# Kernel tuning notes

Hardware: AMD Instinct MI355X
Metric: run time of the kernel (lower is better)

The kernel has to match this reference:

```python
import jax, jax.numpy as jnp
import numpy as np

# Static module hyperparameters (from init_kwargs)
K = 4        # kernel_size
STRIDE = 2
L = 2        # n_layers
F = 4        # filters
NQ = 6       # n_qubits = ceil(log2(4*4*4)) = 6
D = 1 << NQ  # statevector dim = 64 = in_channels*K*K (no padding needed)

# Pauli-Z expectation sign table: wire 0 is the most-significant bit (PennyLane convention)
_bits = (jnp.arange(D)[None, :] >> (NQ - 1 - jnp.arange(NQ)[:, None])) & 1  # (NQ, D)
ZSIGNS = (1 - 2 * _bits).astype(jnp.float32)                                # (NQ, D)


def setup_inputs() -> dict:
    key = jax.random.key(0)
    k1, k2 = jax.random.split(key)
    x = jax.random.normal(k1, (128, 4, 64, 64), dtype=jnp.float32)
    weights = jax.random.normal(k2, (F, L, NQ, 3), dtype=jnp.float32)
    return {"x": x, "weights": weights}


def _rot_mat(phi, theta, omega):
    # qml.Rot = RZ(omega) @ RY(theta) @ RZ(phi)
    c = jnp.cos(theta / 2)
    s = jnp.sin(theta / 2)
    return jnp.stack([
        jnp.stack([jnp.exp(-1j * (phi + omega) / 2) * c, -jnp.exp(1j * (phi - omega) / 2) * s]),
        jnp.stack([jnp.exp(-1j * (phi - omega) / 2) * s, jnp.exp(1j * (phi + omega) / 2) * c]),
    ])  # (2,2) complex64


def _apply_1q(state, U, w):
    # state: (N, D) complex; apply 2x2 unitary on wire w (MSB-first ordering)
    N = state.shape[0]
    s = state.reshape(N, 1 << w, 2, 1 << (NQ - 1 - w))
    s = jnp.einsum('ij,najb->naib', U, s)
    return s.reshape(N, D)


def _apply_cnot(state, c, t):
    # flip target bit t where control bit c is 1
    N = state.shape[0]
    a, b = min(c, t), max(c, t)
    s = state.reshape(N, 1 << a, 2, 1 << (b - a - 1), 2, 1 << (NQ - 1 - b))
    if c < t:
        # control axis=2, target axis=4
        s = s.at[:, :, 1].set(s[:, :, 1, :, ::-1, :])
    else:
        # target axis=2, control axis=4
        s = s.at[:, :, :, :, 1, :].set(s[:, :, ::-1, :, 1, :])
    return s.reshape(N, D)


def _simulate(psi0, wf):
    # psi0: (N, D) complex64 normalized amplitudes; wf: (L, NQ, 3) float32
    state = psi0
    # The torch module applies StronglyEntanglingLayers(weights) L times -> L*L layers total.
    for _ in range(L):
        for l in range(L):
            for w in range(NQ):
                U = _rot_mat(wf[l, w, 0], wf[l, w, 1], wf[l, w, 2])
                state = _apply_1q(state, U, w)
            r = (l % (NQ - 1)) + 1  # StronglyEntanglingLayers default ranges
            for w in range(NQ):
                state = _apply_cnot(state, w, (w + r) % NQ)
    probs = state.real ** 2 + state.imag ** 2  # (N, D)
    return probs @ ZSIGNS.T                    # (N, NQ) Pauli-Z expvals


def reference(x, weights):
    B, C, H, W = x.shape
    oh = (H - K) // STRIDE + 1
    i = jnp.arange(oh) * STRIDE
    # vectorized sliding-window patch extraction, row-major (i outer, j inner)
    rows = x[:, :, i[:, None] + jnp.arange(K)[None, :], :]           # (B,C,oh,K,W)
    pat = rows[:, :, :, :, i[:, None] + jnp.arange(K)[None, :]]      # (B,C,oh,K,oh,K)
    pat = pat.transpose(0, 2, 4, 1, 3, 5).reshape(B, oh * oh, C * K * K)  # (B,P,D), flatten order (C,k,k)
    # AmplitudeEmbedding with normalize=True (C*K*K == 2**NQ, no padding)
    norm = jnp.linalg.norm(pat, axis=-1, keepdims=True)
    psi0 = (pat / norm).astype(jnp.complex64).reshape(-1, D)         # (B*P, D)
    exp = jax.vmap(lambda wf: _simulate(psi0, wf))(weights)          # (F, B*P, NQ)
    out = exp.reshape(F, B, oh * oh, NQ).transpose(1, 0, 3, 2).reshape(B, F * NQ, oh, oh)
    return out
```

## Files before the change

kernel.cpp:

```cpp
#include <hip/hip_runtime.h>

typedef float f32x2 __attribute__((ext_vector_type(2)));
typedef float f32x16 __attribute__((ext_vector_type(16)));
typedef __bf16 bf16x8 __attribute__((ext_vector_type(8)));

static __device__ __forceinline__ unsigned short f2bf(float v) {
    unsigned u = __builtin_bit_cast(unsigned, v);
    unsigned r = (u + 0x7FFFu + ((u >> 16) & 1u)) >> 16;
    return (unsigned short)r;
}
static __device__ __forceinline__ bf16x8 ldg8(const unsigned short* p) {
    uint4 u = *(const uint4*)p;
    return __builtin_bit_cast(bf16x8, u);
}
static __device__ __forceinline__ f32x16 mfma32(bf16x8 a, bf16x8 b, f32x16 c) {
    return __builtin_amdgcn_mfma_f32_32x32x16_bf16(a, b, c, 0, 0, 0);
}

__global__ __launch_bounds__(256) void prep_M(const float* __restrict__ wts,
                                              unsigned short* __restrict__ Mhi) {
    __shared__ float gls[12][8];
    const int f = blockIdx.x >> 4;
    const int tid = threadIdx.x;
    if (tid < 12) {
        int l = tid / 6, w = tid % 6;
        const float* p = wts + ((f * 2 + l) * 6 + w) * 3;
        float phi = p[0], theta = p[1], omega = p[2];
        float c, s; sincosf(0.5f * theta, &s, &c);
        float sapo, capo, samo, camo;
        sincosf(0.5f * (phi + omega), &sapo, &capo);
        sincosf(0.5f * (phi - omega), &samo, &camo);
        float* o = gls[tid];
        o[0] =  capo * c;  o[1] = -sapo * c;
        o[2] = -camo * s;  o[3] = -samo * s;
        o[4] =  camo * s;  o[5] = -samo * s;
        o[6] =  capo * c;  o[7] =  sapo * c;
    }
    __syncthreads();

    const int lane = tid & 63;
    const int wid  = tid >> 6;
    const int bas  = (blockIdx.x & 15) * 4 + wid;

    int src0 = lane, src1 = lane;
#pragma unroll
    for (int w = 5; w >= 0; --w) { int tq = (w + 1) % 6; src0 ^= ((src0 >> (5 - w)) & 1) << (5 - tq); }
#pragma unroll
    for (int w = 5; w >= 0; --w) { int tq = (w + 2) % 6; src1 ^= ((src1 >> (5 - w)) & 1) << (5 - tq); }

    float ar = (lane == bas) ? 1.0f : 0.0f, ai = 0.0f;
#pragma unroll
    for (int rep = 0; rep < 2; ++rep) {
#pragma unroll
        for (int l = 0; l < 2; ++l) {
#pragma unroll
            for (int w = 0; w < 6; ++w) {
                const float* gp = gls[l * 6 + w];
                const float4 uA = *(const float4*)gp;
                const float4 uB = *(const float4*)(gp + 4);
                const int m = 32 >> w;
                const float br = __shfl_xor(ar, m);
                const float bi = __shfl_xor(ai, m);
                const bool hi = (lane & m) != 0;
                const float cmr = hi ? uB.z : uA.x;
                const float cmi = hi ? uB.w : uA.y;
                const float cpr = hi ? uB.x : uA.z;
                const float cpi = hi ? uB.y : uA.w;
                const float nr = cmr * ar - cmi * ai + cpr * br - cpi * bi;
                const float ni = cmr * ai + cmi * ar + cpr * bi + cpi * br;
                ar = nr; ai = ni;
            }
            const int src = l ? src1 : src0;
            ar = __shfl(ar, src);
            ai = __shfl(ai, src);
        }
    }
    Mhi[((f * 2 + 0) * 64 + lane) * 64 + bas] = f2bf(ar);
    Mhi[((f * 2 + 1) * 64 + lane) * 64 + bas] = f2bf(ai);
}

__global__ __launch_bounds__(256, 3) void qconv_main(
        const float* __restrict__ x,
        const unsigned short* __restrict__ Mhi,
        float* __restrict__ out) {
    __shared__ __align__(16) unsigned short psiH[2][4096];
    __shared__ float zbuf[2][6][4][64];

    const int tid  = threadIdx.x;
    const int lane = tid & 63;
    const int w    = tid >> 6;
    const int bid  = blockIdx.x;

    {
        const int p = tid >> 2;
        const int q = tid & 3;
        const int n = bid * 64 + p;
        const int b0 = n / 961, pos = n - b0 * 961;
        const int i = pos / 31, j = pos - i * 31;
        const float* base0 = x + (((b0 * 4 + q) * 64) + i * 2) * 64 + j * 2;
        float v[2][16];
#pragma unroll
        for (int t = 0; t < 2; ++t) {
            const float* base = base0 + t * 64 * 4 * 64 * 64;
#pragma unroll
            for (int kh = 0; kh < 4; ++kh) {
                const float* r = base + kh * 64;
                *(f32x2*)&v[t][kh * 4]     = *(const f32x2*)r;
                *(f32x2*)&v[t][kh * 4 + 2] = *(const f32x2*)(r + 2);
            }
        }
#pragma unroll
        for (int t = 0; t < 2; ++t) {
            float ss = 0.f;
#pragma unroll
            for (int k = 0; k < 16; ++k) ss += v[t][k] * v[t][k];
            ss += __shfl_xor(ss, 1);
            ss += __shfl_xor(ss, 2);
            const float rn = rsqrtf(ss);
            unsigned hu[8];
#pragma unroll
            for (int k2 = 0; k2 < 8; ++k2) {
                __bf16 h0 = (__bf16)(v[t][2 * k2] * rn);
                __bf16 h1 = (__bf16)(v[t][2 * k2 + 1] * rn);
                hu[k2] = (unsigned)__builtin_bit_cast(unsigned short, h0)
                       | ((unsigned)__builtin_bit_cast(unsigned short, h1) << 16);
            }
            const int s0i = p * 64 + ((2 * q) ^ (p & 7)) * 8;
            const int s1i = p * 64 + ((2 * q + 1) ^ (p & 7)) * 8;
            *(uint4*)&psiH[t][s0i] = make_uint4(hu[0], hu[1], hu[2], hu[3]);
            *(uint4*)&psiH[t][s1i] = make_uint4(hu[4], hu[5], hu[6], hu[7]);
        }
    }
    __syncthreads();

    bf16x8 Bh[2][2][4];
    const int pc  = lane & 31;
    const int hi5 = lane >> 5;
#pragma unroll
    for (int t = 0; t < 2; ++t) {
#pragma unroll
        for (int ct = 0; ct < 2; ++ct) {
            const int pp = ct * 32 + pc;
#pragma unroll
            for (int ks = 0; ks < 4; ++ks) {
                const int idx = pp * 64 + ((2 * ks + hi5) ^ (pp & 7)) * 8;
                Bh[t][ct][ks] = __builtin_bit_cast(bf16x8, *(const uint4*)&psiH[t][idx]);
            }
        }
    }

    const int arow = ((lane >> 4) & 1) * 4096 + (w * 16 + (lane & 15)) * 64 + hi5 * 8;

#pragma unroll 1
    for (int f = 0; f < 4; ++f) {
        bf16x8 A[4];
#pragma unroll
        for (int ks = 0; ks < 4; ++ks) A[ks] = ldg8(Mhi + f * 8192 + arow + ks * 16);

        f32x16 C00, C01, C10, C11;
#pragma unroll
        for (int r = 0; r < 16; ++r) { C00[r] = 0.f; C01[r] = 0.f; C10[r] = 0.f; C11[r] = 0.f; }
#pragma unroll
        for (int ks = 0; ks < 4; ++ks) {
            C00 = mfma32(A[ks], Bh[0][0][ks], C00);
            C01 = mfma32(A[ks], Bh[0][1][ks], C01);
            C10 = mfma32(A[ks], Bh[1][0][ks], C10);
            C11 = mfma32(A[ks], Bh[1][1][ks], C11);
        }

#pragma unroll
        for (int t = 0; t < 2; ++t) {
#pragma unroll
            for (int ct = 0; ct < 2; ++ct) {
                const f32x16 Cv = t ? (ct ? C11 : C10) : (ct ? C01 : C00);
                float P[8];
#pragma unroll
                for (int r = 0; r < 8; ++r) P[r] = Cv[r] * Cv[r] + Cv[r + 8] * Cv[r + 8];
                const float e0 = P[0] + P[1], o0 = P[0] - P[1];
                const float e1 = P[2] + P[3], o1 = P[2] - P[3];
                const float e2 = P[4] + P[5], o2 = P[4] - P[5];
                const float e3 = P[6] + P[7], o3 = P[6] - P[7];
                const float s01 = e0 + e1, s23 = e2 + e3;
                float S  = s01 + s23;
                float Z2 = s01 - s23;
                float Z4 = (e0 - e1) + (e2 - e3);
                float Z5 = o0 + o1 + o2 + o3;
                float Z3 = hi5 ? -S : S;
                S  += __shfl_xor(S, 32);
                Z2 += __shfl_xor(Z2, 32);
                Z3 += __shfl_xor(Z3, 32);
                Z4 += __shfl_xor(Z4, 32);
                Z5 += __shfl_xor(Z5, 32);
                if (lane < 32) {
                    const int pp = ct * 32 + lane;
                    zbuf[t][0][w][pp] = (w & 2) ? -S : S;
                    zbuf[t][1][w][pp] = (w & 1) ? -S : S;
                    zbuf[t][2][w][pp] = Z2;
                    zbuf[t][3][w][pp] = Z3;
                    zbuf[t][4][w][pp] = Z4;
                    zbuf[t][5][w][pp] = Z5;
                }
            }
        }
        __syncthreads();

#pragma unroll
        for (int u = tid; u < 768; u += 256) {
            const int t   = u / 384;
            const int rem = u - t * 384;
            const int q   = rem >> 6;
            const int p   = rem & 63;
            const float* zb = &zbuf[t][q][0][p];
            const float sum = zb[0] + zb[64] + zb[128] + zb[192];
            const int nn = bid * 64 + p;
            int bb = nn / 961;
            const int pos = nn - bb * 961;
            bb += t * 64;
            out[(bb * 24 + f * 6 + q) * 961 + pos] = sum;
        }
        __syncthreads();
    }
}

extern "C" void kernel_launch(void* const* d_in, const int* in_sizes, int n_in,
                              void* d_out, int out_size, void* d_ws, size_t ws_size,
                              hipStream_t stream) {
    const float* x   = (const float*)d_in[0];
    const float* wts = (const float*)d_in[1];
    float* out = (float*)d_out;

    unsigned short* Mhi = (unsigned short*)d_ws;

    prep_M<<<64, 256, 0, stream>>>(wts, Mhi);

    qconv_main<<<961, 256, 0, stream>>>(x, Mhi, out);
}
```

Baseline: 30.22 us.

## Prefetch next filter's unitary, double-buffer zbuf, and split MFMA accumulators

Loads the first filter's A fragments before the barrier and prefetches the next filter's A fragments during the current iteration, so global-load latency overlaps with compute. The zbuf reduction buffer is double-buffered by filter parity, which lets the trailing __syncthreads in each loop iteration be dropped. The MFMA accumulators are cut from four to two by computing the two batch halves one after the other, which lowers register pressure. The cost is a larger shared-memory footprint and more live registers for the prefetched fragments.

```diff
diff --git a/kernel.cpp b/kernel.cpp
--- a/kernel.cpp
+++ b/kernel.cpp
@@ -84,7 +84,7 @@
         const unsigned short* __restrict__ Mhi,
         float* __restrict__ out) {
     __shared__ __align__(16) unsigned short psiH[2][4096];
-    __shared__ float zbuf[2][6][4][64];
+    __shared__ float zbuf[2][2][6][4][64];
 
     const int tid  = threadIdx.x;
     const int lane = tid & 63;
@@ -131,11 +131,18 @@
             *(uint4*)&psiH[t][s1i] = make_uint4(hu[4], hu[5], hu[6], hu[7]);
         }
     }
+
+    const int hi5  = lane >> 5;
+    const int arow = ((lane >> 4) & 1) * 4096 + (w * 16 + (lane & 15)) * 64 + hi5 * 8;
+
+    bf16x8 A[4];
+#pragma unroll
+    for (int ks = 0; ks < 4; ++ks) A[ks] = ldg8(Mhi + arow + ks * 16);
+
     __syncthreads();
 
     bf16x8 Bh[2][2][4];
-    const int pc  = lane & 31;
-    const int hi5 = lane >> 5;
+    const int pc = lane & 31;
 #pragma unroll
     for (int t = 0; t < 2; ++t) {
 #pragma unroll
@@ -149,30 +156,38 @@
         }
     }
 
-    const int arow = ((lane >> 4) & 1) * 4096 + (w * 16 + (lane & 15)) * 64 + hi5 * 8;
-
 #pragma unroll 1
     for (int f = 0; f < 4; ++f) {
-        bf16x8 A[4];
-#pragma unroll
-        for (int ks = 0; ks < 4; ++ks) A[ks] = ldg8(Mhi + f * 8192 + arow + ks * 16);
-
-        f32x16 C00, C01, C10, C11;
-#pragma unroll
-        for (int r = 0; r < 16; ++r) { C00[r] = 0.f; C01[r] = 0.f; C10[r] = 0.f; C11[r] = 0.f; }
+        f32x16 C0, C1;
+#pragma unroll
+        for (int r = 0; r < 16; ++r) { C0[r] = 0.f; C1[r] = 0.f; }
 #pragma unroll
         for (int ks = 0; ks < 4; ++ks) {
-            C00 = mfma32(A[ks], Bh[0][0][ks], C00);
-            C01 = mfma32(A[ks], Bh[0][1][ks], C01);
-            C10 = mfma32(A[ks], Bh[1][0][ks], C10);
-            C11 = mfma32(A[ks], Bh[1][1][ks], C11);
+            C0 = mfma32(A[ks], Bh[0][0][ks], C0);
+            C1 = mfma32(A[ks], Bh[0][1][ks], C1);
+        }
+
+        bf16x8 An[4];
+        if (f < 3) {
+#pragma unroll
+            for (int ks = 0; ks < 4; ++ks)
+                An[ks] = ldg8(Mhi + (f + 1) * 8192 + arow + ks * 16);
         }
 
 #pragma unroll
         for (int t = 0; t < 2; ++t) {
+            if (t == 1) {
+#pragma unroll
+                for (int r = 0; r < 16; ++r) { C0[r] = 0.f; C1[r] = 0.f; }
+#pragma unroll
+                for (int ks = 0; ks < 4; ++ks) {
+                    C0 = mfma32(A[ks], Bh[1][0][ks], C0);
+                    C1 = mfma32(A[ks], Bh[1][1][ks], C1);
+                }
+            }
 #pragma unroll
             for (int ct = 0; ct < 2; ++ct) {
-                const f32x16 Cv = t ? (ct ? C11 : C10) : (ct ? C01 : C00);
+                const f32x16 Cv = ct ? C1 : C0;
                 float P[8];
 #pragma unroll
                 for (int r = 0; r < 8; ++r) P[r] = Cv[r] * Cv[r] + Cv[r + 8] * Cv[r + 8];
@@ -193,12 +208,13 @@
                 Z5 += __shfl_xor(Z5, 32);
                 if (lane < 32) {
                     const int pp = ct * 32 + lane;
-                    zbuf[t][0][w][pp] = (w & 2) ? -S : S;
-                    zbuf[t][1][w][pp] = (w & 1) ? -S : S;
-                    zbuf[t][2][w][pp] = Z2;
-                    zbuf[t][3][w][pp] = Z3;
-                    zbuf[t][4][w][pp] = Z4;
-                    zbuf[t][5][w][pp] = Z5;
+                    float* zb = &zbuf[f & 1][t][0][w][pp];
+                    zb[0 * 256] = (w & 2) ? -S : S;
+                    zb[1 * 256] = (w & 1) ? -S : S;
+                    zb[2 * 256] = Z2;
+                    zb[3 * 256] = Z3;
+                    zb[4 * 256] = Z4;
+                    zb[5 * 256] = Z5;
                 }
             }
         }
@@ -210,7 +226,7 @@
             const int rem = u - t * 384;
             const int q   = rem >> 6;
             const int p   = rem & 63;
-            const float* zb = &zbuf[t][q][0][p];
+            const float* zb = &zbuf[f & 1][t][q][0][p];
             const float sum = zb[0] + zb[64] + zb[128] + zb[192];
             const int nn = bid * 64 + p;
             int bb = nn / 961;
@@ -218,7 +234,11 @@
             bb += t * 64;
             out[(bb * 24 + f * 6 + q) * 961 + pos] = sum;
         }
-        __syncthreads();
+
+        if (f < 3) {
+#pragma unroll
+            for (int ks = 0; ks < 4; ++ks) A[ks] = An[ks];
+        }
     }
 }
 
```

Result: slower. 31.02 us (+2.6%).
